# Performance work log

Measured on AMD Instinct MI355X. Metric: run time of the kernel, lower is better.

## Reference

```python
import jax, jax.numpy as jnp
import numpy as np

S, B, D = 2048, 2, 1024          # seq, batch, hidden
E, K = 64, 2                     # num_experts, top_k
I, SI = 512, 512                 # moe_intermediate, shared_expert_intermediate
CAP = 256                        # per-expert capacity; mean load = S*B*K/E = 128, 256 is >16 sigma -> no drops


def setup_inputs() -> dict:
    key = jax.random.key(0)
    ks = jax.random.split(key, 8)
    sc = lambda d: 1.0 / np.sqrt(d)
    return {
        "hidden_states": jax.random.normal(ks[0], (S, B, D), jnp.float32),
        "router_w": jax.random.normal(ks[1], (E, D), jnp.float32) * sc(D),          # FujiTopKRouter.weight
        "gate_up_proj": jax.random.normal(ks[2], (E, 2 * I, D), jnp.float32) * sc(D),
        "down_proj": jax.random.normal(ks[3], (E, D, I), jnp.float32) * sc(I),
        "sh_gate_w": jax.random.normal(ks[4], (SI, D), jnp.float32) * sc(D),
        "sh_up_w": jax.random.normal(ks[5], (SI, D), jnp.float32) * sc(D),
        "sh_down_w": jax.random.normal(ks[6], (D, SI), jnp.float32) * sc(SI),
        "sh_expert_gate_w": jax.random.normal(ks[7], (1, D), jnp.float32) * sc(D),
    }


def _moe(x, router_w, gate_up_proj, down_proj, sh_gate_w, sh_up_w, sh_down_w, sh_expert_gate_w):
    T = x.shape[0]
    # ---- shared expert (SwiGLU) + sigmoid gate ----
    shared = jnp.dot(jax.nn.silu(x @ sh_gate_w.T) * (x @ sh_up_w.T), sh_down_w.T)
    shared = jax.nn.sigmoid(x @ sh_expert_gate_w.T) * shared                      # [T, D]
    # ---- router: softmax (fp32) -> top-k -> normalize ----
    probs = jax.nn.softmax((x @ router_w.T).astype(jnp.float32), axis=-1)         # [T, E]
    top_w, top_i = jax.lax.top_k(probs, K)                                        # [T, K]
    top_w = top_w / (jnp.sum(top_w, axis=-1, keepdims=True) + 1e-9)
    top_w = top_w.astype(x.dtype)
    # ---- dispatch: permute (token, slot) pairs into fixed-capacity expert buffers ----
    e_f = top_i.reshape(-1)                                                       # [T*K] expert id per pair
    w_f = top_w.reshape(-1)                                                       # [T*K]
    tok = jnp.arange(T * K) // K                                                  # [T*K] source token
    oh = jax.nn.one_hot(e_f, E, dtype=jnp.int32)                                  # [T*K, E]
    pos = jnp.sum(jnp.cumsum(oh, axis=0) * oh, axis=-1) - 1                       # slot within expert
    buf = jnp.zeros((E, CAP, D), x.dtype).at[e_f, pos].set(x[tok])                # [E, C, D]
    # ---- per-expert SwiGLU as batched GEMMs ----
    h = jnp.einsum('ecd,eid->eci', buf, gate_up_proj)                             # [E, C, 2I]
    g, u = jnp.split(h, 2, axis=-1)
    y = jnp.einsum('eci,edi->ecd', jax.nn.silu(g) * u, down_proj)                 # [E, C, D]
    # ---- combine: gather back, weight, scatter-add to tokens ----
    routed = jnp.zeros_like(x).at[tok].add(y[e_f, pos] * w_f[:, None])            # [T, D]
    return shared + routed, probs


def reference(hidden_states, router_w, gate_up_proj, down_proj,
              sh_gate_w, sh_up_w, sh_down_w, sh_expert_gate_w):
    s, b, d = hidden_states.shape
    x = hidden_states.reshape(-1, d)
    out, router_logits = _moe(x, router_w, gate_up_proj, down_proj,
                              sh_gate_w, sh_up_w, sh_down_w, sh_expert_gate_w)
    return out.reshape(s, b, d), router_logits
```

## Files before the change

### kernel.cpp

```cpp
#include <hip/hip_runtime.h>
#include <hip/hip_bf16.h>
#include <stdint.h>

#define T_TOK 4096
#define DDIM  1024
#define NEXP  64
#define IDIM  512
#define SIDIM 512
#define CAP   256
#define KZ    8

typedef __attribute__((ext_vector_type(4))) float f32x4;
typedef __attribute__((ext_vector_type(8))) short bf16x8;

__device__ __forceinline__ bf16x8 cvt8(f32x4 a, f32x4 b) {
    union { __hip_bfloat162 h[4]; bf16x8 v; } u;
    u.h[0] = __float22bfloat162_rn(make_float2(a[0], a[1]));
    u.h[1] = __float22bfloat162_rn(make_float2(a[2], a[3]));
    u.h[2] = __float22bfloat162_rn(make_float2(b[0], b[1]));
    u.h[3] = __float22bfloat162_rn(make_float2(b[2], b[3]));
    return u.v;
}
__device__ __forceinline__ short f2bs(float f) {
    union { __hip_bfloat16 h; short s; } u; u.h = __float2bfloat16(f); return u.s;
}

__device__ __forceinline__ void gload16(const void* g, void* l) {
    __builtin_amdgcn_global_load_lds((const __attribute__((address_space(1))) void*)g,
                                     (__attribute__((address_space(3))) void*)l, 16, 0, 0);
}

__device__ __forceinline__ bf16x8 fragbf(const char* base, int row, int sk) {
    return *(const bf16x8*)(base + row * 64 + ((sk ^ ((row >> 1) & 3)) << 4));
}

__global__ __launch_bounds__(256) void cvtw(const float* __restrict__ src,
                                            short* __restrict__ dst, int n8) {
    int i = blockIdx.x * blockDim.x + threadIdx.x;
    int stride = gridDim.x * blockDim.x;
    for (; i < n8; i += stride) {
        f32x4 lo = *(const f32x4*)(src + (size_t)i * 8);
        f32x4 hi = *(const f32x4*)(src + (size_t)i * 8 + 4);
        *(bf16x8*)(dst + (size_t)i * 8) = cvt8(lo, hi);
    }
}

__global__ __launch_bounds__(256) void logits_kernel(const float* __restrict__ X,
                                                     const float* __restrict__ RW,
                                                     float* __restrict__ lpart) {
    __shared__ float sX[64 * 33];
    __shared__ float sW[64 * 33];
    int m0 = blockIdx.x * 64;
    int kz = blockIdx.y;
    int kbase = kz * (DDIM / KZ);
    int tid = threadIdx.x;
    int tg = tid >> 4;
    int eg = tid & 15;
    float acc[4][4] = {};
    for (int k0 = 0; k0 < DDIM / KZ; k0 += 32) {
        __syncthreads();
#pragma unroll
        for (int i = 0; i < 8; ++i) {
            int idx = i * 256 + tid;
            int r = idx >> 5, c = idx & 31;
            sX[r * 33 + c] = X[(size_t)(m0 + r) * DDIM + kbase + k0 + c];
            sW[r * 33 + c] = RW[(size_t)r * DDIM + kbase + k0 + c];
        }
        __syncthreads();
#pragma unroll 4
        for (int k = 0; k < 32; ++k) {
            float xv[4], wv[4];
#pragma unroll
            for (int i = 0; i < 4; ++i) xv[i] = sX[(tg * 4 + i) * 33 + k];
#pragma unroll
            for (int j = 0; j < 4; ++j) wv[j] = sW[(eg * 4 + j) * 33 + k];
#pragma unroll
            for (int i = 0; i < 4; ++i)
#pragma unroll
                for (int j = 0; j < 4; ++j) acc[i][j] += xv[i] * wv[j];
        }
    }
    float* outp = lpart + (size_t)kz * T_TOK * NEXP;
#pragma unroll
    for (int i = 0; i < 4; ++i)
#pragma unroll
        for (int j = 0; j < 4; ++j)
            outp[(size_t)(m0 + tg * 4 + i) * NEXP + eg * 4 + j] = acc[i][j];
}

__global__ __launch_bounds__(256) void topk_kernel(const float* __restrict__ lpart,
                                                   const float* __restrict__ X,
                                                   const float* __restrict__ SEG,
                                                   float* __restrict__ probs_out,
                                                   int* __restrict__ counts,
                                                   int* __restrict__ tok_slot,
                                                   float* __restrict__ w_slot,
                                                   float* __restrict__ gate_sh) {
    int lane = threadIdx.x & 63;
    int wv   = threadIdx.x >> 6;
    int t    = blockIdx.x * 4 + wv;
    size_t li = (size_t)t * NEXP + lane;
    float l = 0.f;
#pragma unroll
    for (int z = 0; z < KZ; ++z) l += lpart[(size_t)z * T_TOK * NEXP + li];
    float mx = l;
    for (int s = 32; s; s >>= 1) mx = fmaxf(mx, __shfl_xor(mx, s));
    float e = __expf(l - mx);
    float sum = e;
    for (int s = 32; s; s >>= 1) sum += __shfl_xor(sum, s);
    float prob = e / sum;
    probs_out[li] = prob;
    float v = prob; int idx = lane;
    for (int s = 32; s; s >>= 1) {
        float ov = __shfl_xor(v, s); int oi = __shfl_xor(idx, s);
        if (ov > v || (ov == v && oi < idx)) { v = ov; idx = oi; }
    }
    float v1 = v; int i1 = idx;
    v = (lane == i1) ? -1e30f : prob; idx = lane;
    for (int s = 32; s; s >>= 1) {
        float ov = __shfl_xor(v, s); int oi = __shfl_xor(idx, s);
        if (ov > v || (ov == v && oi < idx)) { v = ov; idx = oi; }
    }
    float v2 = v; int i2 = idx;
    float denom = v1 + v2 + 1e-9f;
    if (lane == 0) {
        int s1 = atomicAdd(&counts[i1], 1);
        if (s1 < CAP) { tok_slot[i1 * CAP + s1] = t; w_slot[i1 * CAP + s1] = v1 / denom; }
        int s2 = atomicAdd(&counts[i2], 1);
        if (s2 < CAP) { tok_slot[i2 * CAP + s2] = t; w_slot[i2 * CAP + s2] = v2 / denom; }
    }
    float g = 0.f;
    const float* xr = X + (size_t)t * DDIM + lane * 16;
    const float* sr = SEG + lane * 16;
#pragma unroll
    for (int j = 0; j < 4; ++j) {
        f32x4 xv = *(const f32x4*)(xr + j * 4);
        f32x4 sv = *(const f32x4*)(sr + j * 4);
#pragma unroll
        for (int q = 0; q < 4; ++q) g += xv[q] * sv[q];
    }
    for (int s = 32; s; s >>= 1) g += __shfl_xor(g, s);
    if (lane == 0) gate_sh[t] = 1.f / (1.f + __expf(-g));
}

__global__ __launch_bounds__(256) void xgather(const float* __restrict__ X,
                                               const int* __restrict__ counts,
                                               const int* __restrict__ tok_slot,
                                               short* __restrict__ xg,
                                               short* __restrict__ xsh) {
    int b = blockIdx.x, tid = threadIdx.x;
    if (b < 512) {
        int r = b & 7, j = b >> 3;
        int e = (j & 7) * 8 + r;
        int s0 = (j >> 3) * 32;
        int M = counts[e]; if (M > CAP) M = CAP;
        for (int i = tid; i < 32 * 128; i += 256) {
            int sl = s0 + (i >> 7);
            int ch = i & 127;
            int src = (sl < M) ? tok_slot[e * CAP + sl] : 0;
            const float* p = X + (size_t)src * DDIM + ch * 8;
            f32x4 lo = *(const f32x4*)p, hi = *(const f32x4*)(p + 4);
            *(bf16x8*)(xg + ((size_t)e * CAP + sl) * DDIM + ch * 8) = cvt8(lo, hi);
        }
    } else {
        int r0 = (b - 512) * 32;
        for (int i = tid; i < 32 * 128; i += 256) {
            int row = r0 + (i >> 7), ch = i & 127;
            const float* p = X + (size_t)row * DDIM + ch * 8;
            f32x4 lo = *(const f32x4*)p, hi = *(const f32x4*)(p + 4);
            *(bf16x8*)(xsh + (size_t)row * DDIM + ch * 8) = cvt8(lo, hi);
        }
    }
}

__global__ __launch_bounds__(256, 4) void gateup_all(const short* __restrict__ xg,
                                                     const short* __restrict__ xsh,
                                                     const short* __restrict__ gupb,
                                                     const short* __restrict__ sgb,
                                                     const short* __restrict__ subw,
                                                     const int* __restrict__ counts,
                                                     short* __restrict__ act,
                                                     short* __restrict__ act_sh) {
    __shared__ char smem[2 * 16384];
    const int NS = DDIM / 32;
    int f = blockIdx.x;
    bool expert = f < 1024;
    int e = 0, m0, n0, M;
    const short *Wgb, *Wub, *Abase;
    short* act_out;
    size_t out_base, arow0;
    if (expert) {
        int r = f & 7, q = (f >> 3) & 7, n = (f >> 6) & 7, y = f >> 9;
        e = q * 8 + r;
        n0 = n * 64; m0 = y * 128;
        M = counts[e]; if (M > CAP) M = CAP;
        if (m0 >= M) return;
        Wgb = gupb + (size_t)e * (2 * IDIM) * DDIM;
        Wub = Wgb + (size_t)IDIM * DDIM;
        Abase = xg; arow0 = (size_t)e * CAP + m0;
        act_out = act; out_base = (size_t)e * CAP * IDIM;
    } else {
        int g = f - 1024;
        int mp = g & 31, n = g >> 5;
        n0 = n * 64; m0 = mp * 128;
        M = T_TOK; Wgb = sgb; Wub = subw;
        Abase = xsh; arow0 = (size_t)m0;
        act_out = act_sh; out_base = 0;
    }
    int tid = threadIdx.x, lane = tid & 63, wv = tid >> 6;
    int wm = wv >> 1, wn = wv & 1;

    int gsl = (lane & 3) ^ ((lane >> 3) & 3);
    int crow = wv * 16 + (lane >> 2);
    const short* gpA0 = Abase + (arow0 + crow) * DDIM + gsl * 8;
    const short* gpA1 = Abase + (arow0 + crow + 64) * DDIM + gsl * 8;
    const short* gpBg = Wgb + (size_t)(n0 + crow) * DDIM + gsl * 8;
    const short* gpBu = Wub + (size_t)(n0 + crow) * DDIM + gsl * 8;
    int oA0 = wv * 1024, oA1 = (wv + 4) * 1024;
    int oBg = 8192 + wv * 1024, oBu = 12288 + wv * 1024;

    auto issue = [&](int buf, int s) {
        char* base = smem + buf * 16384;
        int k = s * 32;
        gload16(gpA0 + k, base + oA0);
        gload16(gpA1 + k, base + oA1);
        gload16(gpBg + k, base + oBg);
        gload16(gpBu + k, base + oBu);
    };

    int fm = lane & 15, sk = lane >> 4;
    f32x4 accg[4][2] = {}, accu[4][2] = {};
    auto compute = [&](int buf) {
        const char* base = smem + buf * 16384;
        bf16x8 bg[2], bu[2];
#pragma unroll
        for (int nt = 0; nt < 2; ++nt) {
            int row = wn * 32 + nt * 16 + fm;
            bg[nt] = fragbf(base + 8192, row, sk);
            bu[nt] = fragbf(base + 12288, row, sk);
        }
#pragma unroll
        for (int mt = 0; mt < 4; ++mt) {
            bf16x8 a = fragbf(base, wm * 64 + mt * 16 + fm, sk);
#pragma unroll
            for (int nt = 0; nt < 2; ++nt) {
                accg[mt][nt] = __builtin_amdgcn_mfma_f32_16x16x32_bf16(a, bg[nt], accg[mt][nt], 0, 0, 0);
                accu[mt][nt] = __builtin_amdgcn_mfma_f32_16x16x32_bf16(a, bu[nt], accu[mt][nt], 0, 0, 0);
            }
        }
    };

    issue(0, 0);
#pragma unroll 1
    for (int s = 0; s < NS; s += 2) {
        __syncthreads();
        if (s + 1 < NS) issue(1, s + 1);
        compute(0);
        __syncthreads();
        if (s + 2 < NS) issue(0, s + 2);
        compute(1);
    }

    int frow = (lane >> 4) * 4, fcol = lane & 15;
#pragma unroll
    for (int mt = 0; mt < 4; ++mt)
#pragma unroll
        for (int r = 0; r < 4; ++r) {
            int row = m0 + wm * 64 + mt * 16 + frow + r;
            if (row < M) {
#pragma unroll
                for (int nt = 0; nt < 2; ++nt) {
                    float g = accg[mt][nt][r];
                    float u = accu[mt][nt][r];
                    float a = (g / (1.f + __expf(-g))) * u;
                    act_out[out_base + (size_t)row * IDIM + (n0 + wn * 32 + nt * 16 + fcol)] = f2bs(a);
                }
            }
        }
}

__global__ __launch_bounds__(256, 4) void down_all(const short* __restrict__ act,
                                                   const short* __restrict__ act_sh,
                                                   const short* __restrict__ dwb,
                                                   const short* __restrict__ sdb,
                                                   const int* __restrict__ counts,
                                                   const int* __restrict__ tok_slot,
                                                   const float* __restrict__ w_slot,
                                                   const float* __restrict__ gate_sh,
                                                   float* __restrict__ out) {
    __shared__ char smem[2 * 16384];
    const int KD = IDIM;
    const int NS = KD / 32;
    int f = blockIdx.x;
    bool expert = f < 1024;
    int e = 0, m0, n0, M;
    const short *A, *W;
    if (expert) {
        int r = f & 7, q = (f >> 3) & 7, n = (f >> 6) & 7, y = f >> 9;
        e = q * 8 + r;
        n0 = n * 128; m0 = y * 128;
        M = counts[e]; if (M > CAP) M = CAP;
        if (m0 >= M) return;
        A = act + (size_t)e * CAP * IDIM;
        W = dwb + (size_t)e * DDIM * IDIM;
    } else {
        int g = f - 1024;
        int mp = g & 31, n = g >> 5;
        n0 = n * 128; m0 = mp * 128;
        M = T_TOK; A = act_sh; W = sdb;
    }
    int tid = threadIdx.x, lane = tid & 63, wv = tid >> 6;
    int wm = wv >> 1, wn = wv & 1;

    int gsl = (lane & 3) ^ ((lane >> 3) & 3);
    int crow = wv * 16 + (lane >> 2);
    const short* gpA0 = A + (size_t)(m0 + crow) * KD + gsl * 8;
    const short* gpA1 = A + (size_t)(m0 + crow + 64) * KD + gsl * 8;
    const short* gpB0 = W + (size_t)(n0 + crow) * KD + gsl * 8;
    const short* gpB1 = W + (size_t)(n0 + crow + 64) * KD + gsl * 8;
    int oA0 = wv * 1024, oA1 = (wv + 4) * 1024;
    int oB0 = 8192 + wv * 1024, oB1 = 8192 + (wv + 4) * 1024;

    auto issue = [&](int buf, int s) {
        char* base = smem + buf * 16384;
        int k = s * 32;
        gload16(gpA0 + k, base + oA0);
        gload16(gpA1 + k, base + oA1);
        gload16(gpB0 + k, base + oB0);
        gload16(gpB1 + k, base + oB1);
    };

    int fm = lane & 15, sk = lane >> 4;
    f32x4 acc[4][4] = {};
    auto compute = [&](int buf) {
        const char* base = smem + buf * 16384;
        bf16x8 b[4];
#pragma unroll
        for (int nt = 0; nt < 4; ++nt)
            b[nt] = fragbf(base + 8192, wn * 64 + nt * 16 + fm, sk);
#pragma unroll
        for (int mt = 0; mt < 4; ++mt) {
            bf16x8 a = fragbf(base, wm * 64 + mt * 16 + fm, sk);
#pragma unroll
            for (int nt = 0; nt < 4; ++nt)
                acc[mt][nt] = __builtin_amdgcn_mfma_f32_16x16x32_bf16(a, b[nt], acc[mt][nt], 0, 0, 0);
        }
    };

    issue(0, 0);
#pragma unroll 1
    for (int s = 0; s < NS; s += 2) {
        __syncthreads();
        if (s + 1 < NS) issue(1, s + 1);
        compute(0);
        __syncthreads();
        if (s + 2 < NS) issue(0, s + 2);
        compute(1);
    }

    int frow = (lane >> 4) * 4, fcol = lane & 15;
#pragma unroll
    for (int mt = 0; mt < 4; ++mt)
#pragma unroll
        for (int r = 0; r < 4; ++r) {
            int row = m0 + wm * 64 + mt * 16 + frow + r;
            if (row >= M) continue;
            float scale; int trow;
            if (expert) { scale = w_slot[e * CAP + row]; trow = tok_slot[e * CAP + row]; }
            else        { scale = gate_sh[row];          trow = row; }
#pragma unroll
            for (int nt = 0; nt < 4; ++nt) {
                int col = n0 + wn * 64 + nt * 16 + fcol;
                atomicAdd(&out[(size_t)trow * DDIM + col], acc[mt][nt][r] * scale);
            }
        }
}

extern "C" void kernel_launch(void* const* d_in, const int* in_sizes, int n_in,
                              void* d_out, int out_size, void* d_ws, size_t ws_size,
                              hipStream_t stream) {
    const float* X   = (const float*)d_in[0];
    const float* RW  = (const float*)d_in[1];
    const float* GUP = (const float*)d_in[2];
    const float* DW  = (const float*)d_in[3];
    const float* SG  = (const float*)d_in[4];
    const float* SU  = (const float*)d_in[5];
    const float* SD  = (const float*)d_in[6];
    const float* SEG = (const float*)d_in[7];
    float* out = (float*)d_out;

    char* ws = (char*)d_ws;
    size_t off = 0;
    float* lpart    = (float*)(ws + off); off += (size_t)KZ * T_TOK * NEXP * 4;
    int*   counts   = (int*)  (ws + off); off += 1024;
    int*   tok_slot = (int*)  (ws + off); off += (size_t)NEXP * CAP * 4;
    float* w_slot   = (float*)(ws + off); off += (size_t)NEXP * CAP * 4;
    float* gate_sh  = (float*)(ws + off); off += (size_t)T_TOK * 4;
    short* act      = (short*)(ws + off); off += (size_t)NEXP * CAP * IDIM * 2;
    short* act_sh   = (short*)(ws + off); off += (size_t)T_TOK * SIDIM * 2;
    short* xg       = (short*)(ws + off); off += (size_t)NEXP * CAP * DDIM * 2;
    short* xsh      = (short*)(ws + off); off += (size_t)T_TOK * DDIM * 2;
    short* gupb     = (short*)(ws + off); off += (size_t)NEXP * 2 * IDIM * DDIM * 2;
    short* dwb      = (short*)(ws + off); off += (size_t)NEXP * DDIM * IDIM * 2;
    short* sgb      = (short*)(ws + off); off += (size_t)SIDIM * DDIM * 2;
    short* subw     = (short*)(ws + off); off += (size_t)SIDIM * DDIM * 2;
    short* sdb      = (short*)(ws + off); off += (size_t)DDIM * SIDIM * 2;
    (void)ws_size; (void)in_sizes; (void)n_in; (void)out_size;

    hipMemsetAsync(counts, 0, NEXP * sizeof(int), stream);
    hipMemsetAsync(out, 0, (size_t)T_TOK * DDIM * sizeof(float), stream);

    cvtw<<<2048, 256, 0, stream>>>(GUP, gupb, NEXP * 2 * IDIM * DDIM / 8);
    cvtw<<<2048, 256, 0, stream>>>(DW, dwb, NEXP * DDIM * IDIM / 8);
    cvtw<<<256, 256, 0, stream>>>(SG, sgb, SIDIM * DDIM / 8);
    cvtw<<<256, 256, 0, stream>>>(SU, subw, SIDIM * DDIM / 8);
    cvtw<<<256, 256, 0, stream>>>(SD, sdb, DDIM * SIDIM / 8);

    logits_kernel<<<dim3(T_TOK / 64, KZ), 256, 0, stream>>>(X, RW, lpart);
    topk_kernel<<<T_TOK / 4, 256, 0, stream>>>(lpart, X, SEG,
                                               out + (size_t)T_TOK * DDIM,
                                               counts, tok_slot, w_slot, gate_sh);
    xgather<<<640, 256, 0, stream>>>(X, counts, tok_slot, xg, xsh);
    gateup_all<<<1280, 256, 0, stream>>>(xg, xsh, gupb, sgb, subw, counts, act, act_sh);
    down_all<<<1280, 256, 0, stream>>>(act, act_sh, dwb, sdb, counts, tok_slot,
                                       w_slot, gate_sh, out);
}
```

Before: 697.5 us.

## Fuse fp32-to-bf16 weight conversion into GEMM loads and enlarge M tiles

Drops the five separate weight-conversion kernels and their bf16 weight buffers. The gate/up and down GEMMs now stage fp32 weight tiles straight into LDS with a wider XOR swizzle and convert them to bf16 while reading MFMA fragments. Blocks grow to 512 threads with a 256-row M tile, so each expert's whole capacity is covered by one block and each weight tile is read once per expert. The cost is double the LDS (64 KB per block), which lowers occupancy, plus extra conversion work in the inner loop.

```diff
diff --git a/kernel.cpp b/kernel.cpp
--- a/kernel.cpp
+++ b/kernel.cpp
@@ -30,19 +30,15 @@
                                      (__attribute__((address_space(3))) void*)l, 16, 0, 0);
 }
 
+__device__ __forceinline__ bf16x8 frag32(const char* reg0, int row, int s) {
+    const char* p = reg0 + row * 128;
+    int sw = row & 7;
+    f32x4 lo = *(const f32x4*)(p + (((2 * s) ^ sw) << 4));
+    f32x4 hi = *(const f32x4*)(p + (((2 * s + 1) ^ sw) << 4));
+    return cvt8(lo, hi);
+}
 __device__ __forceinline__ bf16x8 fragbf(const char* base, int row, int sk) {
     return *(const bf16x8*)(base + row * 64 + ((sk ^ ((row >> 1) & 3)) << 4));
-}
-
-__global__ __launch_bounds__(256) void cvtw(const float* __restrict__ src,
-                                            short* __restrict__ dst, int n8) {
-    int i = blockIdx.x * blockDim.x + threadIdx.x;
-    int stride = gridDim.x * blockDim.x;
-    for (; i < n8; i += stride) {
-        f32x4 lo = *(const f32x4*)(src + (size_t)i * 8);
-        f32x4 hi = *(const f32x4*)(src + (size_t)i * 8 + 4);
-        *(bf16x8*)(dst + (size_t)i * 8) = cvt8(lo, hi);
-    }
 }
 
 __global__ __launch_bounds__(256) void logits_kernel(const float* __restrict__ X,
@@ -173,71 +169,68 @@
     }
 }
 
-__global__ __launch_bounds__(256, 4) void gateup_all(const short* __restrict__ xg,
+__global__ __launch_bounds__(512, 4) void gateup_all(const short* __restrict__ xg,
                                                      const short* __restrict__ xsh,
-                                                     const short* __restrict__ gupb,
-                                                     const short* __restrict__ sgb,
-                                                     const short* __restrict__ subw,
+                                                     const float* __restrict__ GUP,
+                                                     const float* __restrict__ SG,
+                                                     const float* __restrict__ SU,
                                                      const int* __restrict__ counts,
                                                      short* __restrict__ act,
                                                      short* __restrict__ act_sh) {
-    __shared__ char smem[2 * 16384];
+    __shared__ char smem[2 * 32768];
     const int NS = DDIM / 32;
     int f = blockIdx.x;
-    bool expert = f < 1024;
+    bool expert = f < 512;
     int e = 0, m0, n0, M;
-    const short *Wgb, *Wub, *Abase;
+    const float *Wg, *Wu;
+    const short* Abase;
     short* act_out;
     size_t out_base, arow0;
     if (expert) {
-        int r = f & 7, q = (f >> 3) & 7, n = (f >> 6) & 7, y = f >> 9;
-        e = q * 8 + r;
-        n0 = n * 64; m0 = y * 128;
+        e = ((f >> 3) & 7) * 8 + (f & 7);
+        n0 = (f >> 6) * 64; m0 = 0;
         M = counts[e]; if (M > CAP) M = CAP;
-        if (m0 >= M) return;
-        Wgb = gupb + (size_t)e * (2 * IDIM) * DDIM;
-        Wub = Wgb + (size_t)IDIM * DDIM;
-        Abase = xg; arow0 = (size_t)e * CAP + m0;
+        if (M <= 0) return;
+        Wg = GUP + (size_t)e * (2 * IDIM) * DDIM;
+        Wu = Wg + (size_t)IDIM * DDIM;
+        Abase = xg; arow0 = (size_t)e * CAP;
         act_out = act; out_base = (size_t)e * CAP * IDIM;
     } else {
-        int g = f - 1024;
-        int mp = g & 31, n = g >> 5;
-        n0 = n * 64; m0 = mp * 128;
-        M = T_TOK; Wgb = sgb; Wub = subw;
+        int g = f - 512;
+        m0 = (g & 15) * 256; n0 = (g >> 4) * 64;
+        M = T_TOK; Wg = SG; Wu = SU;
         Abase = xsh; arow0 = (size_t)m0;
         act_out = act_sh; out_base = 0;
     }
     int tid = threadIdx.x, lane = tid & 63, wv = tid >> 6;
     int wm = wv >> 1, wn = wv & 1;
 
-    int gsl = (lane & 3) ^ ((lane >> 3) & 3);
-    int crow = wv * 16 + (lane >> 2);
-    const short* gpA0 = Abase + (arow0 + crow) * DDIM + gsl * 8;
-    const short* gpA1 = Abase + (arow0 + crow + 64) * DDIM + gsl * 8;
-    const short* gpBg = Wgb + (size_t)(n0 + crow) * DDIM + gsl * 8;
-    const short* gpBu = Wub + (size_t)(n0 + crow) * DDIM + gsl * 8;
-    int oA0 = wv * 1024, oA1 = (wv + 4) * 1024;
-    int oBg = 8192 + wv * 1024, oBu = 12288 + wv * 1024;
+    int gslA = (lane & 3) ^ ((lane >> 3) & 3);
+    const short* gpA0 = Abase + (arow0 + wv * 16 + (lane >> 2)) * DDIM + gslA * 8;
+    const short* gpA1 = gpA0 + (size_t)128 * DDIM;
+    int gslB = (lane & 7) ^ ((lane >> 3) & 7);
+    const float* gpBg = Wg + (size_t)(n0 + wv * 8 + (lane >> 3)) * DDIM + gslB * 4;
+    const float* gpBu = Wu + (size_t)(n0 + wv * 8 + (lane >> 3)) * DDIM + gslB * 4;
 
     auto issue = [&](int buf, int s) {
-        char* base = smem + buf * 16384;
+        char* base = smem + buf * 32768;
         int k = s * 32;
-        gload16(gpA0 + k, base + oA0);
-        gload16(gpA1 + k, base + oA1);
-        gload16(gpBg + k, base + oBg);
-        gload16(gpBu + k, base + oBu);
+        gload16(gpA0 + k, base + wv * 1024);
+        gload16(gpA1 + k, base + (wv + 8) * 1024);
+        gload16(gpBg + k, base + 16384 + wv * 1024);
+        gload16(gpBu + k, base + 24576 + wv * 1024);
     };
 
     int fm = lane & 15, sk = lane >> 4;
     f32x4 accg[4][2] = {}, accu[4][2] = {};
     auto compute = [&](int buf) {
-        const char* base = smem + buf * 16384;
+        const char* base = smem + buf * 32768;
         bf16x8 bg[2], bu[2];
 #pragma unroll
         for (int nt = 0; nt < 2; ++nt) {
             int row = wn * 32 + nt * 16 + fm;
-            bg[nt] = fragbf(base + 8192, row, sk);
-            bu[nt] = fragbf(base + 12288, row, sk);
+            bg[nt] = frag32(base + 16384, row, sk);
+            bu[nt] = frag32(base + 24576, row, sk);
         }
 #pragma unroll
         for (int mt = 0; mt < 4; ++mt) {
@@ -267,7 +260,7 @@
 #pragma unroll
         for (int r = 0; r < 4; ++r) {
             int row = m0 + wm * 64 + mt * 16 + frow + r;
-            if (row < M) {
+            if ((expert ? (row) : (row - m0)) < (expert ? M : 256) && row < M) {
 #pragma unroll
                 for (int nt = 0; nt < 2; ++nt) {
                     float g = accg[mt][nt][r];
@@ -279,65 +272,62 @@
         }
 }
 
-__global__ __launch_bounds__(256, 4) void down_all(const short* __restrict__ act,
+__global__ __launch_bounds__(512, 4) void down_all(const short* __restrict__ act,
                                                    const short* __restrict__ act_sh,
-                                                   const short* __restrict__ dwb,
-                                                   const short* __restrict__ sdb,
+                                                   const float* __restrict__ DW,
+                                                   const float* __restrict__ SD,
                                                    const int* __restrict__ counts,
                                                    const int* __restrict__ tok_slot,
                                                    const float* __restrict__ w_slot,
                                                    const float* __restrict__ gate_sh,
                                                    float* __restrict__ out) {
-    __shared__ char smem[2 * 16384];
+    __shared__ char smem[2 * 32768];
     const int KD = IDIM;
     const int NS = KD / 32;
     int f = blockIdx.x;
-    bool expert = f < 1024;
+    bool expert = f < 512;
     int e = 0, m0, n0, M;
-    const short *A, *W;
+    const short* A;
+    const float* W;
     if (expert) {
-        int r = f & 7, q = (f >> 3) & 7, n = (f >> 6) & 7, y = f >> 9;
-        e = q * 8 + r;
-        n0 = n * 128; m0 = y * 128;
+        e = ((f >> 3) & 7) * 8 + (f & 7);
+        n0 = (f >> 6) * 128; m0 = 0;
         M = counts[e]; if (M > CAP) M = CAP;
-        if (m0 >= M) return;
+        if (M <= 0) return;
         A = act + (size_t)e * CAP * IDIM;
-        W = dwb + (size_t)e * DDIM * IDIM;
+        W = DW + (size_t)e * DDIM * IDIM;
     } else {
-        int g = f - 1024;
-        int mp = g & 31, n = g >> 5;
-        n0 = n * 128; m0 = mp * 128;
-        M = T_TOK; A = act_sh; W = sdb;
+        int g = f - 512;
+        m0 = (g & 15) * 256; n0 = (g >> 4) * 128;
+        M = T_TOK; A = act_sh; W = SD;
     }
     int tid = threadIdx.x, lane = tid & 63, wv = tid >> 6;
     int wm = wv >> 1, wn = wv & 1;
 
-    int gsl = (lane & 3) ^ ((lane >> 3) & 3);
-    int crow = wv * 16 + (lane >> 2);
-    const short* gpA0 = A + (size_t)(m0 + crow) * KD + gsl * 8;
-    const short* gpA1 = A + (size_t)(m0 + crow + 64) * KD + gsl * 8;
-    const short* gpB0 = W + (size_t)(n0 + crow) * KD + gsl * 8;
-    const short* gpB1 = W + (size_t)(n0 + crow + 64) * KD + gsl * 8;
-    int oA0 = wv * 1024, oA1 = (wv + 4) * 1024;
-    int oB0 = 8192 + wv * 1024, oB1 = 8192 + (wv + 4) * 1024;
+    int gslA = (lane & 3) ^ ((lane >> 3) & 3);
+    const short* gpA0 = A + (size_t)(m0 + wv * 16 + (lane >> 2)) * KD + gslA * 8;
+    const short* gpA1 = gpA0 + (size_t)128 * KD;
+    int gslB = (lane & 7) ^ ((lane >> 3) & 7);
+    const float* gpB0 = W + (size_t)(n0 + wv * 8 + (lane >> 3)) * KD + gslB * 4;
+    const float* gpB1 = gpB0 + (size_t)64 * KD;
 
     auto issue = [&](int buf, int s) {
-        char* base = smem + buf * 16384;
+        char* base = smem + buf * 32768;
         int k = s * 32;
-        gload16(gpA0 + k, base + oA0);
-        gload16(gpA1 + k, base + oA1);
-        gload16(gpB0 + k, base + oB0);
-        gload16(gpB1 + k, base + oB1);
+        gload16(gpA0 + k, base + wv * 1024);
+        gload16(gpA1 + k, base + (wv + 8) * 1024);
+        gload16(gpB0 + k, base + 16384 + wv * 1024);
+        gload16(gpB1 + k, base + 16384 + (wv + 8) * 1024);
     };
 
     int fm = lane & 15, sk = lane >> 4;
     f32x4 acc[4][4] = {};
     auto compute = [&](int buf) {
-        const char* base = smem + buf * 16384;
+        const char* base = smem + buf * 32768;
         bf16x8 b[4];
 #pragma unroll
         for (int nt = 0; nt < 4; ++nt)
-            b[nt] = fragbf(base + 8192, wn * 64 + nt * 16 + fm, sk);
+            b[nt] = frag32(base + 16384, wn * 64 + nt * 16 + fm, sk);
 #pragma unroll
         for (int mt = 0; mt < 4; ++mt) {
             bf16x8 a = fragbf(base, wm * 64 + mt * 16 + fm, sk);
@@ -363,11 +353,12 @@
     for (int mt = 0; mt < 4; ++mt)
 #pragma unroll
         for (int r = 0; r < 4; ++r) {
-            int row = m0 + wm * 64 + mt * 16 + frow + r;
+            int lrow = wm * 64 + mt * 16 + frow + r;
+            int row = m0 + lrow;
             if (row >= M) continue;
             float scale; int trow;
-            if (expert) { scale = w_slot[e * CAP + row]; trow = tok_slot[e * CAP + row]; }
-            else        { scale = gate_sh[row];          trow = row; }
+            if (expert) { scale = w_slot[e * CAP + lrow]; trow = tok_slot[e * CAP + lrow]; }
+            else        { scale = gate_sh[row];           trow = row; }
 #pragma unroll
             for (int nt = 0; nt < 4; ++nt) {
                 int col = n0 + wn * 64 + nt * 16 + fcol;
@@ -400,28 +391,17 @@
     short* act_sh   = (short*)(ws + off); off += (size_t)T_TOK * SIDIM * 2;
     short* xg       = (short*)(ws + off); off += (size_t)NEXP * CAP * DDIM * 2;
     short* xsh      = (short*)(ws + off); off += (size_t)T_TOK * DDIM * 2;
-    short* gupb     = (short*)(ws + off); off += (size_t)NEXP * 2 * IDIM * DDIM * 2;
-    short* dwb      = (short*)(ws + off); off += (size_t)NEXP * DDIM * IDIM * 2;
-    short* sgb      = (short*)(ws + off); off += (size_t)SIDIM * DDIM * 2;
-    short* subw     = (short*)(ws + off); off += (size_t)SIDIM * DDIM * 2;
-    short* sdb      = (short*)(ws + off); off += (size_t)DDIM * SIDIM * 2;
     (void)ws_size; (void)in_sizes; (void)n_in; (void)out_size;
 
     hipMemsetAsync(counts, 0, NEXP * sizeof(int), stream);
     hipMemsetAsync(out, 0, (size_t)T_TOK * DDIM * sizeof(float), stream);
-
-    cvtw<<<2048, 256, 0, stream>>>(GUP, gupb, NEXP * 2 * IDIM * DDIM / 8);
-    cvtw<<<2048, 256, 0, stream>>>(DW, dwb, NEXP * DDIM * IDIM / 8);
-    cvtw<<<256, 256, 0, stream>>>(SG, sgb, SIDIM * DDIM / 8);
-    cvtw<<<256, 256, 0, stream>>>(SU, subw, SIDIM * DDIM / 8);
-    cvtw<<<256, 256, 0, stream>>>(SD, sdb, DDIM * SIDIM / 8);
 
     logits_kernel<<<dim3(T_TOK / 64, KZ), 256, 0, stream>>>(X, RW, lpart);
     topk_kernel<<<T_TOK / 4, 256, 0, stream>>>(lpart, X, SEG,
                                                out + (size_t)T_TOK * DDIM,
                                                counts, tok_slot, w_slot, gate_sh);
     xgather<<<640, 256, 0, stream>>>(X, counts, tok_slot, xg, xsh);
-    gateup_all<<<1280, 256, 0, stream>>>(xg, xsh, gupb, sgb, subw, counts, act, act_sh);
-    down_all<<<1280, 256, 0, stream>>>(act, act_sh, dwb, sdb, counts, tok_slot,
-                                       w_slot, gate_sh, out);
-}
+    gateup_all<<<640, 512, 0, stream>>>(xg, xsh, GUP, SG, SU, counts, act, act_sh);
+    down_all<<<640, 512, 0, stream>>>(act, act_sh, DW, SD, counts, tok_slot,
+                                      w_slot, gate_sh, out);
+}
```

After: 660.1 us. 5.4% less time.
